# Kernel tuning notes

Measured on AMD Instinct MI355X. Metric: run time of the kernel, lower is better.

## Reference

```python
import jax, jax.numpy as jnp
import numpy as np

NEG_SLOPE = 0.01  # torch F.leaky_relu default

N_NODES = 100000
N_EDGES = 1250000
N_REL = 10
D = 64


def setup_inputs() -> dict:
    key = jax.random.key(0)
    ks = jax.random.split(key, 8)
    return {
        "nfeat": jax.random.normal(ks[0], (N_NODES, D), dtype=jnp.float32),
        "efeat": jax.random.normal(ks[1], (N_EDGES, D), dtype=jnp.float32),
        "relation_weight": jax.random.normal(ks[2], (N_REL, D, D), dtype=jnp.float32) * (1.0 / np.sqrt(D)),
        "res_fc_w": jax.random.normal(ks[3], (D, D), dtype=jnp.float32) * (1.0 / np.sqrt(D)),
        "res_fc2_w": jax.random.normal(ks[4], (D, D), dtype=jnp.float32) * (1.0 / np.sqrt(D)),
        "src": jax.random.randint(ks[5], (N_EDGES,), 0, N_NODES, dtype=jnp.int32),
        "dst": jnp.sort(jax.random.randint(ks[6], (N_EDGES,), 0, N_NODES, dtype=jnp.int32)),
        "etype": jax.random.randint(ks[7], (N_EDGES,), 0, N_REL, dtype=jnp.int32),
    }


def reference(nfeat, efeat, relation_weight, res_fc_w, res_fc2_w, src, dst, etype):
    # KGAT conv (eval mode, feat_drop=0):
    #   t_r = W_{r(e)} h_src,  h_r = W_{r(e)} h_dst
    #   att = <t_r, tanh(h_r + e_r)>  per edge
    #   a   = edge_softmax over incoming edges of dst
    #   h_neighbor[v] = sum_{e: dst=v} a_e * h_src
    #   h' = leaky_relu((h + h_nb) W1^T) + leaky_relu((h * h_nb) W2^T)
    n = nfeat.shape[0]
    # Project every node by every relation once (N*R*D), instead of
    # materializing a per-edge [E, D, D] weight gather.
    proj = jnp.einsum('ni,rio->nro', nfeat, relation_weight)  # [N, R, D]
    t_r = proj[src, etype]   # [E, D]
    h_r = proj[dst, etype]   # [E, D]
    att = jnp.sum(t_r * jnp.tanh(h_r + efeat), axis=-1)  # [E]

    # segment softmax over dst (edge_softmax)
    seg_max = jax.ops.segment_max(att, dst, num_segments=n)  # [N]
    ex = jnp.exp(att - seg_max[dst])
    seg_sum = jax.ops.segment_sum(ex, dst, num_segments=n)   # [N]
    a = ex / seg_sum[dst]                                    # [E]

    # weighted scatter-sum aggregation of src features
    h_nb = jax.ops.segment_sum(nfeat[src] * a[:, None], dst, num_segments=n)  # [N, D]

    out = (jax.nn.leaky_relu((nfeat + h_nb) @ res_fc_w.T, NEG_SLOPE)
           + jax.nn.leaky_relu((nfeat * h_nb) @ res_fc2_w.T, NEG_SLOPE))
    return out
```

## Files before the change

kernel.cpp:

```cpp
#include <hip/hip_runtime.h>
#include <hip/hip_fp16.h>
#include <math.h>

#define D 64
#define WAVE 64

typedef _Float16 f16;
typedef f16 f16x8 __attribute__((ext_vector_type(8)));
typedef float f32x4 __attribute__((ext_vector_type(4)));

__device__ __forceinline__ float wave_reduce_sum(float v) {
    v += __shfl_xor(v, 32);
    v += __shfl_xor(v, 16);
    v += __shfl_xor(v, 8);
    v += __shfl_xor(v, 4);
    v += __shfl_xor(v, 2);
    v += __shfl_xor(v, 1);
    return v;
}

__device__ __forceinline__ float wave_reduce_max(float v) {
    v = fmaxf(v, __shfl_xor(v, 32));
    v = fmaxf(v, __shfl_xor(v, 16));
    v = fmaxf(v, __shfl_xor(v, 8));
    v = fmaxf(v, __shfl_xor(v, 4));
    v = fmaxf(v, __shfl_xor(v, 2));
    v = fmaxf(v, __shfl_xor(v, 1));
    return v;
}

__device__ __forceinline__ float fast_tanh(float x) {
    float e = __expf(2.0f * x);
    return 1.0f - 2.0f / (e + 1.0f);
}

__global__ void wt_kernel(const float* __restrict__ W, f16* __restrict__ WT,
                          int n_rel) {
    int idx = blockIdx.x * blockDim.x + threadIdx.x;
    if (idx >= n_rel * D * D) return;
    int r = idx >> 12;
    int rem = idx & 4095;
    int o = rem >> 6;
    int k = rem & 63;
    WT[idx] = (f16)W[((size_t)r << 12) + (k << 6) + o];
}

__global__ __launch_bounds__(256) void proj_kernel(
    const float* __restrict__ nfeat, const f16* __restrict__ WT,
    f16* __restrict__ proj, int n_nodes, int n_rel) {
    __shared__ f16 Al[64 * D];
    const int tid = threadIdx.x;
    const int lane = tid & 63;
    const int wid = tid >> 6;
    const int n0 = blockIdx.x * 64;

    {
        const float4* g4 = (const float4*)(nfeat + (size_t)n0 * D);
        int avail_rows = n_nodes - n0;
        if (avail_rows > 64) avail_rows = 64;
        const int avail4 = avail_rows * (D / 4);
#pragma unroll
        for (int i = tid; i < 64 * (D / 4); i += 256) {
            float4 v = (i < avail4) ? g4[i] : make_float4(0.f, 0.f, 0.f, 0.f);
            f16* dp = &Al[i * 4];
            dp[0] = (f16)v.x; dp[1] = (f16)v.y; dp[2] = (f16)v.z; dp[3] = (f16)v.w;
        }
    }
    __syncthreads();

    const int g = lane >> 4;
    const int c = lane & 15;
    const int arow = wid * 16 + c;
    f16x8 a0 = *(const f16x8*)&Al[arow * D + g * 8];
    f16x8 a1 = *(const f16x8*)&Al[arow * D + 32 + g * 8];

    const int row_base = n0 + wid * 16 + g * 4;

    for (int r = 0; r < n_rel; ++r) {
        const f16* Wb = WT + ((size_t)r << 12);
        f32x4 acc[4] = {{0.f,0.f,0.f,0.f},{0.f,0.f,0.f,0.f},
                        {0.f,0.f,0.f,0.f},{0.f,0.f,0.f,0.f}};
#pragma unroll
        for (int t = 0; t < 4; ++t) {
            const f16* bp = Wb + (size_t)(t * 16 + c) * D + g * 8;
            f16x8 b0 = *(const f16x8*)bp;
            f16x8 b1 = *(const f16x8*)(bp + 32);
            acc[t] = __builtin_amdgcn_mfma_f32_16x16x32_f16(a0, b0, acc[t], 0, 0, 0);
            acc[t] = __builtin_amdgcn_mfma_f32_16x16x32_f16(a1, b1, acc[t], 0, 0, 0);
        }
#pragma unroll
        for (int t = 0; t < 4; ++t) {
#pragma unroll
            for (int j = 0; j < 4; ++j) {
                int n = row_base + j;
                if (n < n_nodes)
                    proj[((size_t)n * n_rel + r) * D + t * 16 + c] = (f16)acc[t][j];
            }
        }
    }
}

__global__ __launch_bounds__(256) void att_kernel(
    const __half* __restrict__ proj, const float* __restrict__ efeat,
    const int* __restrict__ src, const int* __restrict__ dst,
    const int* __restrict__ etype, float* __restrict__ att,
    int n_edges, int n_rel) {
    const int lane = threadIdx.x & 63;
    const int wid = threadIdx.x >> 6;
    const int g = lane >> 4;
    const int c4 = lane & 15;

    int e = (blockIdx.x * 4 + wid) * 4 + g;
    const bool valid = e < n_edges;
    const int ec = valid ? e : (n_edges - 1);
    const int s = src[ec];
    const int d = dst[ec];
    const int et = etype[ec];

    const float4* ef4 = (const float4*)(efeat + (size_t)ec * D);
    float4 ef = ef4[c4];
    const __half2* tp = (const __half2*)(proj + ((size_t)s * n_rel + et) * D) + c4 * 2;
    const __half2* hp = (const __half2*)(proj + ((size_t)d * n_rel + et) * D) + c4 * 2;
    float2 tA = __half22float2(tp[0]);
    float2 tB = __half22float2(tp[1]);
    float2 hA = __half22float2(hp[0]);
    float2 hB = __half22float2(hp[1]);

    float v = tA.x * fast_tanh(hA.x + ef.x)
            + tA.y * fast_tanh(hA.y + ef.y)
            + tB.x * fast_tanh(hB.x + ef.z)
            + tB.y * fast_tanh(hB.y + ef.w);
    v += __shfl_xor(v, 8);
    v += __shfl_xor(v, 4);
    v += __shfl_xor(v, 2);
    v += __shfl_xor(v, 1);
    if (valid && c4 == 0) att[e] = v;
}

__global__ void rowptr_kernel(const int* __restrict__ dst, int* __restrict__ row_ptr,
                              int n_edges, int n_nodes) {
    int tid = blockIdx.x * blockDim.x + threadIdx.x;
    int stride = gridDim.x * blockDim.x;
    for (int e = tid; e < n_edges; e += stride) {
        int d = dst[e];
        int dprev = (e == 0) ? -1 : dst[e - 1];
        for (int v = dprev + 1; v <= d; ++v) row_ptr[v] = e;
    }
    if (tid == 0) {
        int dlast = dst[n_edges - 1];
        for (int v = dlast + 1; v <= n_nodes; ++v) row_ptr[v] = n_edges;
    }
}

__global__ __launch_bounds__(256) void agg_kernel(
    const float* __restrict__ att, const int* __restrict__ src,
    const int* __restrict__ row_ptr, const float* __restrict__ nfeat,
    float* __restrict__ h_nb, int n_nodes) {
    const int lane = threadIdx.x & 63;
    const int wid = __builtin_amdgcn_readfirstlane(threadIdx.x >> 6);
    const int n = blockIdx.x * 4 + wid;
    if (n >= n_nodes) return;
    const int s = row_ptr[n];
    const int t = row_ptr[n + 1];
    float a0 = 0.0f, a1 = 0.0f, a2 = 0.0f, a3 = 0.0f;
    float inv = 0.0f;
    if (t > s) {
        float m = -INFINITY;
        for (int base = s; base < t; base += WAVE) {
            int idx = base + lane;
            float a = (idx < t) ? att[idx] : -INFINITY;
            m = fmaxf(m, a);
        }
        m = wave_reduce_max(m);
        float exsum = 0.0f;
        for (int base = s; base < t; base += WAVE) {
            int idx = base + lane;
            float ex = (idx < t) ? __expf(att[idx] - m) : 0.0f;
            int sv = (idx < t) ? src[idx] : 0;
            exsum += ex;
            int cnt = t - base;
            if (cnt > WAVE) cnt = WAVE;
            int cnt4 = (cnt + 3) & ~3;
            for (int j = 0; j < cnt4; j += 4) {
                float c0 = __shfl(ex, j + 0); int s0 = __shfl(sv, j + 0);
                float c1 = __shfl(ex, j + 1); int s1 = __shfl(sv, j + 1);
                float c2 = __shfl(ex, j + 2); int s2 = __shfl(sv, j + 2);
                float c3 = __shfl(ex, j + 3); int s3 = __shfl(sv, j + 3);
                a0 = fmaf(c0, nfeat[(size_t)s0 * D + lane], a0);
                a1 = fmaf(c1, nfeat[(size_t)s1 * D + lane], a1);
                a2 = fmaf(c2, nfeat[(size_t)s2 * D + lane], a2);
                a3 = fmaf(c3, nfeat[(size_t)s3 * D + lane], a3);
            }
        }
        float ssum = wave_reduce_sum(exsum);
        inv = 1.0f / ssum;
    }
    h_nb[(size_t)n * D + lane] = ((a0 + a1) + (a2 + a3)) * inv;
}

__global__ __launch_bounds__(256) void out_kernel(
    const float* __restrict__ nfeat, const float* h_nb,
    const float* __restrict__ W1, const float* __restrict__ W2,
    float* out, int n_nodes) {
    const int lane = threadIdx.x & 63;
    const int wid = __builtin_amdgcn_readfirstlane(threadIdx.x >> 6);
    float w1[D], w2[D];
#pragma unroll
    for (int i = 0; i < D; ++i) w1[i] = W1[lane * D + i];
#pragma unroll
    for (int i = 0; i < D; ++i) w2[i] = W2[lane * D + i];
    const int nwaves = gridDim.x * 4;
    for (int n = blockIdx.x * 4 + wid; n < n_nodes; n += nwaves) {
        const int nn = __builtin_amdgcn_readfirstlane(n);
        const float* x = nfeat + (size_t)nn * D;
        const float* h = h_nb + (size_t)nn * D;
        float a0 = 0.0f, a1 = 0.0f, b0 = 0.0f, b1 = 0.0f;
#pragma unroll
        for (int i = 0; i < D; i += 2) {
            float x0 = x[i], h0 = h[i];
            float x1 = x[i + 1], h1 = h[i + 1];
            a0 = fmaf(x0 + h0, w1[i], a0);
            b0 = fmaf(x0 * h0, w2[i], b0);
            a1 = fmaf(x1 + h1, w1[i + 1], a1);
            b1 = fmaf(x1 * h1, w2[i + 1], b1);
        }
        float a = a0 + a1, b = b0 + b1;
        a = (a > 0.0f) ? a : 0.01f * a;
        b = (b > 0.0f) ? b : 0.01f * b;
        out[(size_t)nn * D + lane] = a + b;
    }
}

extern "C" void kernel_launch(void* const* d_in, const int* in_sizes, int n_in,
                              void* d_out, int out_size, void* d_ws, size_t ws_size,
                              hipStream_t stream) {
    const float* nfeat = (const float*)d_in[0];
    const float* efeat = (const float*)d_in[1];
    const float* relw  = (const float*)d_in[2];
    const float* w1    = (const float*)d_in[3];
    const float* w2    = (const float*)d_in[4];
    const int*   src   = (const int*)d_in[5];
    const int*   dst   = (const int*)d_in[6];
    const int*   etype = (const int*)d_in[7];
    float* out = (float*)d_out;

    const int n_nodes = in_sizes[0] / D;
    const int n_edges = in_sizes[5];
    const int n_rel   = in_sizes[2] / (D * D);

    const size_t ALIGN = 256;
    const size_t proj_bytes = ((size_t)n_nodes * n_rel * D * sizeof(f16) + ALIGN - 1) & ~(ALIGN - 1);
    const size_t att_bytes  = ((size_t)n_edges * sizeof(float) + ALIGN - 1) & ~(ALIGN - 1);
    const size_t rp_bytes   = ((size_t)(n_nodes + 1) * sizeof(int) + ALIGN - 1) & ~(ALIGN - 1);

    float* h_nb = out;

    char* ws = (char*)d_ws;
    f16*  proj    = (f16*)ws;
    float* att    = (float*)(ws + proj_bytes);
    int* row_ptr  = (int*)(ws + proj_bytes + att_bytes);
    f16*  wt      = (f16*)(ws + proj_bytes + att_bytes + rp_bytes);

    rowptr_kernel<<<1024, 256, 0, stream>>>(dst, row_ptr, n_edges, n_nodes);

    wt_kernel<<<(n_rel * D * D + 255) / 256, 256, 0, stream>>>(relw, wt, n_rel);

    proj_kernel<<<(n_nodes + 63) / 64, 256, 0, stream>>>(nfeat, wt, proj,
                                                         n_nodes, n_rel);

    att_kernel<<<(n_edges + 15) / 16, 256, 0, stream>>>((const __half*)proj, efeat,
                                                        src, dst, etype,
                                                        att, n_edges, n_rel);

    agg_kernel<<<(n_nodes + 3) / 4, 256, 0, stream>>>(att, src, row_ptr, nfeat,
                                                      h_nb, n_nodes);

    out_kernel<<<1024, 256, 0, stream>>>(nfeat, h_nb, w1, w2, out, n_nodes);
}
```

Before: 695.4 us.

## Fuse attention and aggregation into one online-softmax kernel per destination node

Removes the separate per-edge attention kernel and the att buffer, and computes attention scores, online softmax and weighted aggregation in a single wave-per-node kernel. The proj kernel also writes an fp16 copy of node features, which the fused kernel gathers instead of fp32 nfeat to halve gather bytes. The out kernel grid grows from 1024 to 3200 blocks. In exchange, each wave handles edges four at a time with full 64-lane shuffle reductions, so edge parallelism is limited for low-degree nodes, and fp16 features reduce precision in the aggregation.

```diff
diff --git a/kernel.cpp b/kernel.cpp
--- a/kernel.cpp
+++ b/kernel.cpp
@@ -8,26 +8,6 @@
 typedef _Float16 f16;
 typedef f16 f16x8 __attribute__((ext_vector_type(8)));
 typedef float f32x4 __attribute__((ext_vector_type(4)));
-
-__device__ __forceinline__ float wave_reduce_sum(float v) {
-    v += __shfl_xor(v, 32);
-    v += __shfl_xor(v, 16);
-    v += __shfl_xor(v, 8);
-    v += __shfl_xor(v, 4);
-    v += __shfl_xor(v, 2);
-    v += __shfl_xor(v, 1);
-    return v;
-}
-
-__device__ __forceinline__ float wave_reduce_max(float v) {
-    v = fmaxf(v, __shfl_xor(v, 32));
-    v = fmaxf(v, __shfl_xor(v, 16));
-    v = fmaxf(v, __shfl_xor(v, 8));
-    v = fmaxf(v, __shfl_xor(v, 4));
-    v = fmaxf(v, __shfl_xor(v, 2));
-    v = fmaxf(v, __shfl_xor(v, 1));
-    return v;
-}
 
 __device__ __forceinline__ float fast_tanh(float x) {
     float e = __expf(2.0f * x);
@@ -47,7 +27,7 @@
 
 __global__ __launch_bounds__(256) void proj_kernel(
     const float* __restrict__ nfeat, const f16* __restrict__ WT,
-    f16* __restrict__ proj, int n_nodes, int n_rel) {
+    f16* __restrict__ proj, f16* __restrict__ nf16, int n_nodes, int n_rel) {
     __shared__ f16 Al[64 * D];
     const int tid = threadIdx.x;
     const int lane = tid & 63;
@@ -62,8 +42,13 @@
 #pragma unroll
         for (int i = tid; i < 64 * (D / 4); i += 256) {
             float4 v = (i < avail4) ? g4[i] : make_float4(0.f, 0.f, 0.f, 0.f);
+            f16 h0 = (f16)v.x, h1 = (f16)v.y, h2 = (f16)v.z, h3 = (f16)v.w;
             f16* dp = &Al[i * 4];
-            dp[0] = (f16)v.x; dp[1] = (f16)v.y; dp[2] = (f16)v.z; dp[3] = (f16)v.w;
+            dp[0] = h0; dp[1] = h1; dp[2] = h2; dp[3] = h3;
+            if (i < avail4) {
+                f16* np = nf16 + (size_t)n0 * D + i * 4;
+                np[0] = h0; np[1] = h1; np[2] = h2; np[3] = h3;
+            }
         }
     }
     __syncthreads();
@@ -98,43 +83,6 @@
             }
         }
     }
-}
-
-__global__ __launch_bounds__(256) void att_kernel(
-    const __half* __restrict__ proj, const float* __restrict__ efeat,
-    const int* __restrict__ src, const int* __restrict__ dst,
-    const int* __restrict__ etype, float* __restrict__ att,
-    int n_edges, int n_rel) {
-    const int lane = threadIdx.x & 63;
-    const int wid = threadIdx.x >> 6;
-    const int g = lane >> 4;
-    const int c4 = lane & 15;
-
-    int e = (blockIdx.x * 4 + wid) * 4 + g;
-    const bool valid = e < n_edges;
-    const int ec = valid ? e : (n_edges - 1);
-    const int s = src[ec];
-    const int d = dst[ec];
-    const int et = etype[ec];
-
-    const float4* ef4 = (const float4*)(efeat + (size_t)ec * D);
-    float4 ef = ef4[c4];
-    const __half2* tp = (const __half2*)(proj + ((size_t)s * n_rel + et) * D) + c4 * 2;
-    const __half2* hp = (const __half2*)(proj + ((size_t)d * n_rel + et) * D) + c4 * 2;
-    float2 tA = __half22float2(tp[0]);
-    float2 tB = __half22float2(tp[1]);
-    float2 hA = __half22float2(hp[0]);
-    float2 hB = __half22float2(hp[1]);
-
-    float v = tA.x * fast_tanh(hA.x + ef.x)
-            + tA.y * fast_tanh(hA.y + ef.y)
-            + tB.x * fast_tanh(hB.x + ef.z)
-            + tB.y * fast_tanh(hB.y + ef.w);
-    v += __shfl_xor(v, 8);
-    v += __shfl_xor(v, 4);
-    v += __shfl_xor(v, 2);
-    v += __shfl_xor(v, 1);
-    if (valid && c4 == 0) att[e] = v;
 }
 
 __global__ void rowptr_kernel(const int* __restrict__ dst, int* __restrict__ row_ptr,
@@ -152,50 +100,85 @@
     }
 }
 
-__global__ __launch_bounds__(256) void agg_kernel(
-    const float* __restrict__ att, const int* __restrict__ src,
-    const int* __restrict__ row_ptr, const float* __restrict__ nfeat,
-    float* __restrict__ h_nb, int n_nodes) {
+__global__ __launch_bounds__(256) void attagg_kernel(
+    const f16* __restrict__ proj, const float* __restrict__ efeat,
+    const int* __restrict__ src, const int* __restrict__ etype,
+    const int* __restrict__ row_ptr, const f16* __restrict__ nf16,
+    float* __restrict__ h_nb, int n_nodes, int n_rel) {
     const int lane = threadIdx.x & 63;
     const int wid = __builtin_amdgcn_readfirstlane(threadIdx.x >> 6);
     const int n = blockIdx.x * 4 + wid;
     if (n >= n_nodes) return;
     const int s = row_ptr[n];
     const int t = row_ptr[n + 1];
-    float a0 = 0.0f, a1 = 0.0f, a2 = 0.0f, a3 = 0.0f;
-    float inv = 0.0f;
-    if (t > s) {
-        float m = -INFINITY;
-        for (int base = s; base < t; base += WAVE) {
-            int idx = base + lane;
-            float a = (idx < t) ? att[idx] : -INFINITY;
-            m = fmaxf(m, a);
-        }
-        m = wave_reduce_max(m);
-        float exsum = 0.0f;
-        for (int base = s; base < t; base += WAVE) {
-            int idx = base + lane;
-            float ex = (idx < t) ? __expf(att[idx] - m) : 0.0f;
-            int sv = (idx < t) ? src[idx] : 0;
-            exsum += ex;
-            int cnt = t - base;
-            if (cnt > WAVE) cnt = WAVE;
-            int cnt4 = (cnt + 3) & ~3;
-            for (int j = 0; j < cnt4; j += 4) {
-                float c0 = __shfl(ex, j + 0); int s0 = __shfl(sv, j + 0);
-                float c1 = __shfl(ex, j + 1); int s1 = __shfl(sv, j + 1);
-                float c2 = __shfl(ex, j + 2); int s2 = __shfl(sv, j + 2);
-                float c3 = __shfl(ex, j + 3); int s3 = __shfl(sv, j + 3);
-                a0 = fmaf(c0, nfeat[(size_t)s0 * D + lane], a0);
-                a1 = fmaf(c1, nfeat[(size_t)s1 * D + lane], a1);
-                a2 = fmaf(c2, nfeat[(size_t)s2 * D + lane], a2);
-                a3 = fmaf(c3, nfeat[(size_t)s3 * D + lane], a3);
-            }
-        }
-        float ssum = wave_reduce_sum(exsum);
-        inv = 1.0f / ssum;
-    }
-    h_nb[(size_t)n * D + lane] = ((a0 + a1) + (a2 + a3)) * inv;
+
+    float m = -INFINITY;
+    float l = 0.0f;
+    float acc = 0.0f;
+    const size_t hbase = (size_t)n * n_rel;
+
+    for (int base = s; base < t; base += 4) {
+        const int tm1 = t - 1;
+        const int e0 = base;
+        const int e1 = (base + 1 < t) ? base + 1 : tm1;
+        const int e2 = (base + 2 < t) ? base + 2 : tm1;
+        const int e3 = (base + 3 < t) ? base + 3 : tm1;
+        const bool p1 = base + 1 < t, p2 = base + 2 < t, p3 = base + 3 < t;
+
+        const int s0 = src[e0], s1 = src[e1], s2 = src[e2], s3 = src[e3];
+        const int q0 = etype[e0], q1 = etype[e1], q2 = etype[e2], q3 = etype[e3];
+
+        float tr0 = (float)proj[((size_t)s0 * n_rel + q0) * D + lane];
+        float tr1 = (float)proj[((size_t)s1 * n_rel + q1) * D + lane];
+        float tr2 = (float)proj[((size_t)s2 * n_rel + q2) * D + lane];
+        float tr3 = (float)proj[((size_t)s3 * n_rel + q3) * D + lane];
+        float nf0 = (float)nf16[(size_t)s0 * D + lane];
+        float nf1 = (float)nf16[(size_t)s1 * D + lane];
+        float nf2 = (float)nf16[(size_t)s2 * D + lane];
+        float nf3 = (float)nf16[(size_t)s3 * D + lane];
+        float ef0 = efeat[(size_t)e0 * D + lane];
+        float ef1 = efeat[(size_t)e1 * D + lane];
+        float ef2 = efeat[(size_t)e2 * D + lane];
+        float ef3 = efeat[(size_t)e3 * D + lane];
+        float hr0 = (float)proj[(hbase + q0) * D + lane];
+        float hr1 = (float)proj[(hbase + q1) * D + lane];
+        float hr2 = (float)proj[(hbase + q2) * D + lane];
+        float hr3 = (float)proj[(hbase + q3) * D + lane];
+
+        float v0 = tr0 * fast_tanh(hr0 + ef0);
+        float v1 = tr1 * fast_tanh(hr1 + ef1);
+        float v2 = tr2 * fast_tanh(hr2 + ef2);
+        float v3 = tr3 * fast_tanh(hr3 + ef3);
+
+#pragma unroll
+        for (int st = 32; st >= 1; st >>= 1) {
+            v0 += __shfl_xor(v0, st);
+            v1 += __shfl_xor(v1, st);
+            v2 += __shfl_xor(v2, st);
+            v3 += __shfl_xor(v3, st);
+        }
+        float a0 = v0;
+        float a1 = p1 ? v1 : -INFINITY;
+        float a2 = p2 ? v2 : -INFINITY;
+        float a3 = p3 ? v3 : -INFINITY;
+
+        float cm = fmaxf(fmaxf(a0, a1), fmaxf(a2, a3));
+        float mn = fmaxf(m, cm);
+        float sc = __expf(m - mn);
+        acc *= sc;
+        l *= sc;
+        float w0 = __expf(a0 - mn);
+        float w1 = __expf(a1 - mn);
+        float w2 = __expf(a2 - mn);
+        float w3 = __expf(a3 - mn);
+        l += (w0 + w1) + (w2 + w3);
+        acc = fmaf(w0, nf0, acc);
+        acc = fmaf(w1, nf1, acc);
+        acc = fmaf(w2, nf2, acc);
+        acc = fmaf(w3, nf3, acc);
+        m = mn;
+    }
+    h_nb[(size_t)n * D + lane] = (l > 0.0f) ? acc / l : 0.0f;
 }
 
 __global__ __launch_bounds__(256) void out_kernel(
@@ -250,30 +233,27 @@
 
     const size_t ALIGN = 256;
     const size_t proj_bytes = ((size_t)n_nodes * n_rel * D * sizeof(f16) + ALIGN - 1) & ~(ALIGN - 1);
-    const size_t att_bytes  = ((size_t)n_edges * sizeof(float) + ALIGN - 1) & ~(ALIGN - 1);
     const size_t rp_bytes   = ((size_t)(n_nodes + 1) * sizeof(int) + ALIGN - 1) & ~(ALIGN - 1);
+    const size_t wt_bytes   = ((size_t)n_rel * D * D * sizeof(f16) + ALIGN - 1) & ~(ALIGN - 1);
 
     float* h_nb = out;
 
     char* ws = (char*)d_ws;
     f16*  proj    = (f16*)ws;
-    float* att    = (float*)(ws + proj_bytes);
-    int* row_ptr  = (int*)(ws + proj_bytes + att_bytes);
-    f16*  wt      = (f16*)(ws + proj_bytes + att_bytes + rp_bytes);
+    int* row_ptr  = (int*)(ws + proj_bytes);
+    f16*  wt      = (f16*)(ws + proj_bytes + rp_bytes);
+    f16*  nf16    = (f16*)(ws + proj_bytes + rp_bytes + wt_bytes);
 
     rowptr_kernel<<<1024, 256, 0, stream>>>(dst, row_ptr, n_edges, n_nodes);
 
     wt_kernel<<<(n_rel * D * D + 255) / 256, 256, 0, stream>>>(relw, wt, n_rel);
 
-    proj_kernel<<<(n_nodes + 63) / 64, 256, 0, stream>>>(nfeat, wt, proj,
+    proj_kernel<<<(n_nodes + 63) / 64, 256, 0, stream>>>(nfeat, wt, proj, nf16,
                                                          n_nodes, n_rel);
 
-    att_kernel<<<(n_edges + 15) / 16, 256, 0, stream>>>((const __half*)proj, efeat,
-                                                        src, dst, etype,
-                                                        att, n_edges, n_rel);
-
-    agg_kernel<<<(n_nodes + 3) / 4, 256, 0, stream>>>(att, src, row_ptr, nfeat,
-                                                      h_nb, n_nodes);
-
-    out_kernel<<<1024, 256, 0, stream>>>(nfeat, h_nb, w1, w2, out, n_nodes);
-}
+    attagg_kernel<<<(n_nodes + 3) / 4, 256, 0, stream>>>(proj, efeat, src, etype,
+                                                         row_ptr, nf16, h_nb,
+                                                         n_nodes, n_rel);
+
+    out_kernel<<<3200, 256, 0, stream>>>(nfeat, h_nb, w1, w2, out, n_nodes);
+}
```

After: 713.1 us. 2.5% more time.
